# Optimization experiments

Hardware: AMD Instinct MI355X
Metric: run time of the kernel (lower is better)

Reference implementation:

```python
import jax, jax.numpy as jnp
import numpy as np

D_MODEL, N_HEADS = 1024, 16
HEAD_DIM = D_MODEL // N_HEADS  # 64
BS, Q_LEN, SEQ_LEN = 4, 1024, 1024


def setup_inputs() -> dict:
    key = jax.random.key(0)
    kq, kk, kv, kp, km = jax.random.split(key, 5)
    q = jax.random.normal(kq, (BS, N_HEADS, Q_LEN, HEAD_DIM), dtype=jnp.float32)
    k = jax.random.normal(kk, (BS, N_HEADS, HEAD_DIM, SEQ_LEN), dtype=jnp.float32)
    v = jax.random.normal(kv, (BS, N_HEADS, SEQ_LEN, HEAD_DIM), dtype=jnp.float32)
    prev = jax.random.normal(kp, (BS, N_HEADS, Q_LEN, SEQ_LEN), dtype=jnp.float32)
    attn_weighted_mask = jax.random.uniform(km, (1, N_HEADS, Q_LEN, SEQ_LEN), dtype=jnp.float32)
    scale = jnp.asarray(HEAD_DIM ** (-0.5), dtype=jnp.float32)  # nn.Parameter scalar
    return {"q": q, "k": k, "v": v, "prev": prev,
            "attn_weighted_mask": attn_weighted_mask, "scale": scale}


def reference(q, k, v, prev, attn_weighted_mask, scale):
    # scores = (q @ k) * scale + prev       [bs, h, q_len, seq_len]
    attn_scores = jnp.einsum('bhqd,bhds->bhqs', q, k) * scale + prev
    # softmax over keys; attn_dropout p=0.0 -> identity
    attn_weights = jax.nn.softmax(attn_scores, axis=-1)
    # post-softmax elementwise weighted mask
    attn_weights = attn_weights * attn_weighted_mask
    # output = attn_weights @ v             [bs, h, q_len, d_v]
    output = jnp.einsum('bhqs,bhsd->bhqd', attn_weights, v)
    # res_attention=True -> also return weights and pre-softmax scores
    return output, attn_weights, attn_scores
```

## Files before the change

kernel.cpp:

```cpp
#include <hip/hip_runtime.h>


#define QL 1024
#define SL 1024
#define HD 64

typedef __attribute__((ext_vector_type(8))) short bf16x8;
typedef __attribute__((ext_vector_type(4))) short bf16x4;
typedef __attribute__((ext_vector_type(4))) float f32x4;

__device__ __forceinline__ short f2bf(float f) {
    union { float f; unsigned u; } v; v.f = f;
    unsigned r = v.u + 0x7FFFu + ((v.u >> 16) & 1u);
    return (short)(r >> 16);
}

__global__ __launch_bounds__(256) void _prepack_kv(
    const float* __restrict__ k, const float* __restrict__ v,
    short* __restrict__ ws)
{
    __shared__ short tile[64][72];
    const int t = threadIdx.x;
    int b = blockIdx.x;
    const float* src; short* dst; int ld_src, ld_dst;
    if (b < 1024) {
        const int bh = b >> 4, st = b & 15;
        src = k + (size_t)bh * 65536 + st * 64;               ld_src = 1024;
        dst = ws + (size_t)bh * 65536 + (size_t)st * 4096;    ld_dst = 64;
    } else {
        b -= 1024;
        const int bh = b >> 4, st = b & 15;
        src = v + (size_t)bh * 65536 + (size_t)st * 4096;     ld_src = 64;
        dst = ws + 4194304 + (size_t)bh * 65536 + st * 64;    ld_dst = 1024;
    }
    {
        const int r = t >> 2, c0 = (t & 3) * 16;
#pragma unroll
        for (int i = 0; i < 4; ++i) {
            float4 f = *(const float4*)&src[(size_t)r * ld_src + c0 + 4 * i];
            bf16x4 s4 = { f2bf(f.x), f2bf(f.y), f2bf(f.z), f2bf(f.w) };
            *(bf16x4*)&tile[r][c0 + 4 * i] = s4;
        }
    }
    __syncthreads();
    {
        const int r = t >> 2, c0 = (t & 3) * 16;
        bf16x8 o0, o1;
#pragma unroll
        for (int j = 0; j < 8; ++j) o0[j] = tile[c0 + j][r];
#pragma unroll
        for (int j = 0; j < 8; ++j) o1[j] = tile[c0 + 8 + j][r];
        *(bf16x8*)&dst[(size_t)r * ld_dst + c0]     = o0;
        *(bf16x8*)&dst[(size_t)r * ld_dst + c0 + 8] = o1;
    }
}

__global__ __launch_bounds__(512, 4) void _attn_main(
    const float* __restrict__ q, const float* __restrict__ prev,
    const float* __restrict__ mask, const float* __restrict__ scale_p,
    const short* __restrict__ Kt, const short* __restrict__ Vt,
    float* __restrict__ out)
{
    __shared__ short wbuf[16384];
    __shared__ float red[128];
    __shared__ float obuf[1024];

    const int tid  = threadIdx.x;
    const int w    = tid >> 6;
    const int lane = tid & 63;
    const int quad = lane >> 4;
    const int lp   = lane & 15;

    const int j   = blockIdx.x;
    const int xcd = j & 7;
    const int i6  = j >> 3;
    const int bh  = xcd * 8 + (i6 >> 3);
    const int sub = i6 & 7;
    const int h   = bh & 15;

    const float scale = scale_p[0];

    const float* Qbh = q    + (size_t)bh * QL * HD;
    const float* Pbh = prev + (size_t)bh * QL * SL;
    const float* Mbh = mask + (size_t)h  * QL * SL;
    const short* Kb  = Kt + (size_t)bh * (SL * HD);
    const short* Vb  = Vt + (size_t)bh * (SL * HD);

    float* Obh = out            + (size_t)bh * QL * HD;
    float* Wbh = out + 4194304  + (size_t)bh * QL * SL;
    float* Sbh = out + 71303168 + (size_t)bh * QL * SL;

    const int s0   = 128 * w;
    const int sq   = s0 + quad * 4;
    const int dgrp = w & 3;
    const int kh   = w >> 2;

    f32x4 accA[8], accB[8];
    float4 qrA[4], qrB[4];

    {
        const int q0 = (sub * 8) * 16;
        const float* pp = Pbh + (size_t)(q0 + lp) * SL + sq;
#pragma unroll
        for (int t = 0; t < 8; ++t) accA[t] = *(const f32x4*)(pp + 16 * t);
        const float* qp = Qbh + (size_t)(q0 + lp) * HD + quad * 8;
        qrA[0] = *(const float4*)qp;        qrA[1] = *(const float4*)(qp + 4);
        qrA[2] = *(const float4*)(qp + 32); qrA[3] = *(const float4*)(qp + 36);
    }

    auto body = [&](f32x4 (&acc)[8], f32x4 (&accN)[8],
                    float4 (&qr)[4], float4 (&qrN)[4], int i) {
        const int q0  = (sub * 8 + i) * 16;
        const int iN  = (i < 7) ? i + 1 : i;
        const int q0N = (sub * 8 + iN) * 16;

        bf16x8 aq0, aq1;
        aq0[0] = f2bf(qr[0].x * scale); aq0[1] = f2bf(qr[0].y * scale);
        aq0[2] = f2bf(qr[0].z * scale); aq0[3] = f2bf(qr[0].w * scale);
        aq0[4] = f2bf(qr[1].x * scale); aq0[5] = f2bf(qr[1].y * scale);
        aq0[6] = f2bf(qr[1].z * scale); aq0[7] = f2bf(qr[1].w * scale);
        aq1[0] = f2bf(qr[2].x * scale); aq1[1] = f2bf(qr[2].y * scale);
        aq1[2] = f2bf(qr[2].z * scale); aq1[3] = f2bf(qr[2].w * scale);
        aq1[4] = f2bf(qr[3].x * scale); aq1[5] = f2bf(qr[3].y * scale);
        aq1[6] = f2bf(qr[3].z * scale); aq1[7] = f2bf(qr[3].w * scale);

#pragma unroll
        for (int t = 0; t < 8; ++t) {
            bf16x8 bk = *(const bf16x8*)&Kb[(size_t)(s0 + 16 * t + lp) * HD + quad * 8];
            acc[t] = __builtin_amdgcn_mfma_f32_16x16x32_bf16(bk, aq0, acc[t], 0, 0, 0);
        }
#pragma unroll
        for (int t = 0; t < 8; ++t) {
            bf16x8 bk = *(const bf16x8*)&Kb[(size_t)(s0 + 16 * t + lp) * HD + 32 + quad * 8];
            acc[t] = __builtin_amdgcn_mfma_f32_16x16x32_bf16(bk, aq1, acc[t], 0, 0, 0);
        }

        {
            float* sp = Sbh + (size_t)(q0 + lp) * SL + sq;
#pragma unroll
            for (int t = 0; t < 8; ++t) *(f32x4*)(sp + 16 * t) = acc[t];
        }

        {
            const float* pp = Pbh + (size_t)(q0N + lp) * SL + sq;
#pragma unroll
            for (int t = 0; t < 8; ++t) accN[t] = *(const f32x4*)(pp + 16 * t);
            const float* qp = Qbh + (size_t)(q0N + lp) * HD + quad * 8;
            qrN[0] = *(const float4*)qp;        qrN[1] = *(const float4*)(qp + 4);
            qrN[2] = *(const float4*)(qp + 32); qrN[3] = *(const float4*)(qp + 36);
        }

        float lsum = 0.f;
#pragma unroll
        for (int t = 0; t < 8; ++t) {
#pragma unroll
            for (int r = 0; r < 4; ++r) {
                float e = __expf(acc[t][r]);
                acc[t][r] = e;
                lsum += e;
            }
        }

        const float* mp = Mbh + (size_t)(q0 + lp) * SL + sq;
        float4 mkA[4];
#pragma unroll
        for (int t = 0; t < 4; ++t) mkA[t] = *(const float4*)(mp + 16 * t);

        lsum += __shfl_xor(lsum, 16);
        lsum += __shfl_xor(lsum, 32);
        if (lane < 16) red[w * 16 + lane] = lsum;
        __syncthreads();
        float rsum = 0.f;
#pragma unroll
        for (int u = 0; u < 8; ++u) rsum += red[u * 16 + lp];
        const float rinv = 1.0f / rsum;

        float4 mkB[4];
#pragma unroll
        for (int t = 0; t < 4; ++t) mkB[t] = *(const float4*)(mp + 64 + 16 * t);

        {
            float* wp = Wbh + (size_t)(q0 + lp) * SL + sq;
#pragma unroll
            for (int t = 0; t < 8; ++t) {
                float4 m4 = (t < 4) ? mkA[t] : mkB[t - 4];
                f32x4 wv;
#pragma unroll
                for (int r = 0; r < 4; ++r) wv[r] = acc[t][r] * rinv * m4[r];
                *(f32x4*)(wp + 16 * t) = wv;
                const int sb = sq + 16 * t;
                bf16x4 wb = { f2bf(wv[0]), f2bf(wv[1]), f2bf(wv[2]), f2bf(wv[3]) };
                *(bf16x4*)&wbuf[((sb >> 3) * 16 + lp) * 8 + (sb & 4)] = wb;
            }
        }
        __syncthreads();

        f32x4 oacc = {0.f, 0.f, 0.f, 0.f};
#pragma unroll 8
        for (int kk = 0; kk < 16; ++kk) {
            const int ks = kh * 16 + kk;
            bf16x8 aw = *(const bf16x8*)&wbuf[((ks * 4 + quad) * 16 + lp) * 8];
            bf16x8 bv = *(const bf16x8*)&Vb[(size_t)(16 * dgrp + lp) * SL
                                            + ks * 32 + quad * 8];
            oacc = __builtin_amdgcn_mfma_f32_16x16x32_bf16(bv, aw, oacc, 0, 0, 0);
        }
        if (kh == 1) {
            *(f32x4*)&obuf[lp * 64 + 16 * dgrp + quad * 4] = oacc;
        }
        __syncthreads();
        if (kh == 0) {
            f32x4 ov = *(const f32x4*)&obuf[lp * 64 + 16 * dgrp + quad * 4];
#pragma unroll
            for (int r = 0; r < 4; ++r) ov[r] += oacc[r];
            *(f32x4*)&Obh[(size_t)(q0 + lp) * HD + 16 * dgrp + quad * 4] = ov;
        }
    };

    for (int ii = 0; ii < 8; ii += 2) {
        body(accA, accB, qrA, qrB, ii);
        body(accB, accA, qrB, qrA, ii + 1);
    }
}

__global__ __launch_bounds__(256) void _attn_fallback(
    const float* __restrict__ q, const float* __restrict__ k,
    const float* __restrict__ v, const float* __restrict__ prev,
    const float* __restrict__ mask, const float* __restrict__ scale_p,
    float* __restrict__ out)
{
    const int WSTR = SL + 8;
    __shared__ short wbuf[16 * (SL + 8)];
    __shared__ float red[4 * 16];

    const int tid  = threadIdx.x;
    const int w    = tid >> 6;
    const int lane = tid & 63;
    const int quad = lane >> 4;
    const int lp   = lane & 15;

    const int blk = blockIdx.x;
    const int bh  = blk >> 6;
    const int qt  = blk & 63;
    const int h   = bh & 15;
    const int q0  = qt * 16;

    const float scale = scale_p[0];

    const float* Qb = q    + (size_t)bh * QL * HD + (size_t)q0 * HD;
    const float* Kb = k    + (size_t)bh * HD * SL;
    const float* Vb = v    + (size_t)bh * SL * HD;
    const float* Pb = prev + (size_t)bh * QL * SL + (size_t)q0 * SL;
    const float* Mb = mask + (size_t)h  * QL * SL + (size_t)q0 * SL;

    float* Ob   = out            + (size_t)bh * QL * HD + (size_t)q0 * HD;
    float* Wout = out + 4194304  + (size_t)bh * QL * SL + (size_t)q0 * SL;
    float* Sout = out + 71303168 + (size_t)bh * QL * SL + (size_t)q0 * SL;

    bf16x8 aq[2];
#pragma unroll
    for (int ks = 0; ks < 2; ++ks) {
        const float* qp = Qb + (size_t)lp * HD + ks * 32 + quad * 8;
#pragma unroll
        for (int j = 0; j < 8; ++j) aq[ks][j] = f2bf(qp[j] * scale);
    }

    const int s0 = 256 * w;
    f32x4 acc[16];
#pragma unroll
    for (int t = 0; t < 16; ++t) {
#pragma unroll
        for (int r = 0; r < 4; ++r)
            acc[t][r] = Pb[(size_t)(quad * 4 + r) * SL + s0 + 16 * t + lp];
    }
#pragma unroll
    for (int ks = 0; ks < 2; ++ks) {
#pragma unroll
        for (int t = 0; t < 16; ++t) {
            bf16x8 bk;
            const float* kp = Kb + (size_t)(ks * 32 + quad * 8) * SL + s0 + 16 * t + lp;
#pragma unroll
            for (int j = 0; j < 8; ++j) bk[j] = f2bf(kp[(size_t)j * SL]);
            acc[t] = __builtin_amdgcn_mfma_f32_16x16x32_bf16(aq[ks], bk, acc[t], 0, 0, 0);
        }
    }

    float lsum[4] = {0.f, 0.f, 0.f, 0.f};
#pragma unroll
    for (int t = 0; t < 16; ++t) {
#pragma unroll
        for (int r = 0; r < 4; ++r) {
            float sv = acc[t][r];
            Sout[(size_t)(quad * 4 + r) * SL + s0 + 16 * t + lp] = sv;
            float e = __expf(sv);
            acc[t][r] = e;
            lsum[r] += e;
        }
    }
#pragma unroll
    for (int r = 0; r < 4; ++r) {
        float s = lsum[r];
        s += __shfl_xor(s, 1);  s += __shfl_xor(s, 2);
        s += __shfl_xor(s, 4);  s += __shfl_xor(s, 8);
        lsum[r] = s;
    }
    if (lp == 0) {
#pragma unroll
        for (int r = 0; r < 4; ++r) red[w * 16 + quad * 4 + r] = lsum[r];
    }
    __syncthreads();
    float rinv[4];
#pragma unroll
    for (int r = 0; r < 4; ++r) {
        float s = red[0 * 16 + quad * 4 + r] + red[1 * 16 + quad * 4 + r]
                + red[2 * 16 + quad * 4 + r] + red[3 * 16 + quad * 4 + r];
        rinv[r] = 1.0f / s;
    }

#pragma unroll
    for (int t = 0; t < 16; ++t) {
#pragma unroll
        for (int r = 0; r < 4; ++r) {
            int row = quad * 4 + r;
            int col = s0 + 16 * t + lp;
            float wv = acc[t][r] * rinv[r] * Mb[(size_t)row * SL + col];
            Wout[(size_t)row * SL + col] = wv;
            wbuf[row * WSTR + col] = f2bf(wv);
        }
    }
    __syncthreads();

    f32x4 oacc = {0.f, 0.f, 0.f, 0.f};
#pragma unroll 4
    for (int ks = 0; ks < 32; ++ks) {
        bf16x8 aw = *(const bf16x8*)&wbuf[lp * WSTR + ks * 32 + quad * 8];
        bf16x8 bv;
        const float* vp = Vb + (size_t)(ks * 32 + quad * 8) * HD + 16 * w + lp;
#pragma unroll
        for (int j = 0; j < 8; ++j) bv[j] = f2bf(vp[(size_t)j * HD]);
        oacc = __builtin_amdgcn_mfma_f32_16x16x32_bf16(aw, bv, oacc, 0, 0, 0);
    }
#pragma unroll
    for (int r = 0; r < 4; ++r)
        Ob[(size_t)(quad * 4 + r) * HD + 16 * w + lp] = oacc[r];
}

extern "C" void kernel_launch(void* const* d_in, const int* in_sizes, int n_in,
                              void* d_out, int out_size, void* d_ws, size_t ws_size,
                              hipStream_t stream) {
    const float* q     = (const float*)d_in[0];
    const float* k     = (const float*)d_in[1];
    const float* v     = (const float*)d_in[2];
    const float* prev  = (const float*)d_in[3];
    const float* mask  = (const float*)d_in[4];
    const float* scale = (const float*)d_in[5];
    float* out = (float*)d_out;

    if (d_ws != nullptr && ws_size >= (size_t)16 * 1024 * 1024) {
        short* ws = (short*)d_ws;
        _prepack_kv<<<dim3(2048), dim3(256), 0, stream>>>(k, v, ws);
        _attn_main<<<dim3(512), dim3(512), 0, stream>>>(
            q, prev, mask, scale, ws, ws + 4194304, out);
    } else {
        _attn_fallback<<<dim3(4096), dim3(256), 0, stream>>>(
            q, k, v, prev, mask, scale, out);
    }
}
```

Baseline: 978.6 us.

## Remap blocks to heads per XCD, hoist mask loads, use LDS-only barriers

Changes the block-to-(batch, head) mapping so that blocks on the same XCD share a head and can reuse its mask rows in L2. Issues all mask loads before the next-tile prefetch, with a scheduling barrier to keep that order, and skips the redundant prefetch on the last iteration. Replaces __syncthreads with a barrier that waits only on LDS counters, so outstanding global loads and stores are no longer drained at each sync. The narrower barrier relies on correct waitcnt handling for global data used after the barrier.

```diff
diff --git a/kernel.cpp b/kernel.cpp
--- a/kernel.cpp
+++ b/kernel.cpp
@@ -14,6 +14,11 @@
     unsigned r = v.u + 0x7FFFu + ((v.u >> 16) & 1u);
     return (short)(r >> 16);
 }
+
+#define LDS_BAR() do {                                        \
+    asm volatile("s_waitcnt lgkmcnt(0)" ::: "memory");        \
+    __builtin_amdgcn_s_barrier();                             \
+} while (0)
 
 __global__ __launch_bounds__(256) void _prepack_kv(
     const float* __restrict__ k, const float* __restrict__ v,
@@ -72,11 +77,12 @@
     const int lp   = lane & 15;
 
     const int j   = blockIdx.x;
-    const int xcd = j & 7;
-    const int i6  = j >> 3;
-    const int bh  = xcd * 8 + (i6 >> 3);
-    const int sub = i6 & 7;
-    const int h   = bh & 15;
+    const int c   = j & 7;
+    const int m   = j >> 3;
+    const int sub = m & 7;
+    const int b   = m >> 4;
+    const int h   = ((m >> 3) & 1) * 8 + c;
+    const int bh  = b * 16 + h;
 
     const float scale = scale_p[0];
 
@@ -111,8 +117,7 @@
     auto body = [&](f32x4 (&acc)[8], f32x4 (&accN)[8],
                     float4 (&qr)[4], float4 (&qrN)[4], int i) {
         const int q0  = (sub * 8 + i) * 16;
-        const int iN  = (i < 7) ? i + 1 : i;
-        const int q0N = (sub * 8 + iN) * 16;
+        const int q0N = q0 + 16;
 
         bf16x8 aq0, aq1;
         aq0[0] = f2bf(qr[0].x * scale); aq0[1] = f2bf(qr[0].y * scale);
@@ -141,7 +146,16 @@
             for (int t = 0; t < 8; ++t) *(f32x4*)(sp + 16 * t) = acc[t];
         }
 
-        {
+        const float* mp = Mbh + (size_t)(q0 + lp) * SL + sq;
+        float4 mkA[4], mkB[4];
+#pragma unroll
+        for (int t = 0; t < 4; ++t) mkA[t] = *(const float4*)(mp + 16 * t);
+#pragma unroll
+        for (int t = 0; t < 4; ++t) mkB[t] = *(const float4*)(mp + 64 + 16 * t);
+
+        __builtin_amdgcn_sched_barrier(0);
+
+        if (i < 7) {
             const float* pp = Pbh + (size_t)(q0N + lp) * SL + sq;
 #pragma unroll
             for (int t = 0; t < 8; ++t) accN[t] = *(const f32x4*)(pp + 16 * t);
@@ -161,23 +175,14 @@
             }
         }
 
-        const float* mp = Mbh + (size_t)(q0 + lp) * SL + sq;
-        float4 mkA[4];
-#pragma unroll
-        for (int t = 0; t < 4; ++t) mkA[t] = *(const float4*)(mp + 16 * t);
-
         lsum += __shfl_xor(lsum, 16);
         lsum += __shfl_xor(lsum, 32);
         if (lane < 16) red[w * 16 + lane] = lsum;
-        __syncthreads();
+        LDS_BAR();
         float rsum = 0.f;
 #pragma unroll
         for (int u = 0; u < 8; ++u) rsum += red[u * 16 + lp];
         const float rinv = 1.0f / rsum;
-
-        float4 mkB[4];
-#pragma unroll
-        for (int t = 0; t < 4; ++t) mkB[t] = *(const float4*)(mp + 64 + 16 * t);
 
         {
             float* wp = Wbh + (size_t)(q0 + lp) * SL + sq;
@@ -193,7 +198,7 @@
                 *(bf16x4*)&wbuf[((sb >> 3) * 16 + lp) * 8 + (sb & 4)] = wb;
             }
         }
-        __syncthreads();
+        LDS_BAR();
 
         f32x4 oacc = {0.f, 0.f, 0.f, 0.f};
 #pragma unroll 8
@@ -207,7 +212,7 @@
         if (kh == 1) {
             *(f32x4*)&obuf[lp * 64 + 16 * dgrp + quad * 4] = oacc;
         }
-        __syncthreads();
+        LDS_BAR();
         if (kh == 0) {
             f32x4 ov = *(const f32x4*)&obuf[lp * 64 + 16 * dgrp + quad * 4];
 #pragma unroll
```

Measured after the change: 1.047 ms. 1.07x slower.

## Remap blocks to share mask tiles across batches and reuse loaded mask rows

Applied to the files above, without the earlier changes.

Changes the block-to-work mapping so each block handles one head and two 16-row query tiles across all four batch elements, instead of eight query tiles of a single (batch, head). The mask tile depends only on head and query rows, so it is now loaded once per query tile and reused for the four batches, cutting mask reads about fourfold. The cost is keeping the mask values in registers across iterations, which raises register pressure under the 512x4 launch bounds. Per-iteration K/V pointers also switch between batches, which may reduce L2 locality for K and V.

```diff
diff --git a/kernel.cpp b/kernel.cpp
--- a/kernel.cpp
+++ b/kernel.cpp
@@ -72,23 +72,14 @@
     const int lp   = lane & 15;
 
     const int j   = blockIdx.x;
-    const int xcd = j & 7;
-    const int i6  = j >> 3;
-    const int bh  = xcd * 8 + (i6 >> 3);
-    const int sub = i6 & 7;
-    const int h   = bh & 15;
+    const int c   = j & 7;
+    const int r   = j >> 3;
+    const int h   = c + 8 * (r & 1);
+    const int q0b = (r >> 1) * 32;
 
     const float scale = scale_p[0];
 
-    const float* Qbh = q    + (size_t)bh * QL * HD;
-    const float* Pbh = prev + (size_t)bh * QL * SL;
-    const float* Mbh = mask + (size_t)h  * QL * SL;
-    const short* Kb  = Kt + (size_t)bh * (SL * HD);
-    const short* Vb  = Vt + (size_t)bh * (SL * HD);
-
-    float* Obh = out            + (size_t)bh * QL * HD;
-    float* Wbh = out + 4194304  + (size_t)bh * QL * SL;
-    float* Sbh = out + 71303168 + (size_t)bh * QL * SL;
+    const float* Mbh = mask + (size_t)h * QL * SL;
 
     const int s0   = 128 * w;
     const int sq   = s0 + quad * 4;
@@ -97,22 +88,29 @@
 
     f32x4 accA[8], accB[8];
     float4 qrA[4], qrB[4];
+    float4 mkA[4], mkB[4];
 
     {
-        const int q0 = (sub * 8) * 16;
-        const float* pp = Pbh + (size_t)(q0 + lp) * SL + sq;
+        const int bh0 = h;
+        const float* pp = prev + (size_t)bh0 * QL * SL + (size_t)(q0b + lp) * SL + sq;
 #pragma unroll
         for (int t = 0; t < 8; ++t) accA[t] = *(const f32x4*)(pp + 16 * t);
-        const float* qp = Qbh + (size_t)(q0 + lp) * HD + quad * 8;
+        const float* qp = q + (size_t)bh0 * QL * HD + (size_t)(q0b + lp) * HD + quad * 8;
         qrA[0] = *(const float4*)qp;        qrA[1] = *(const float4*)(qp + 4);
         qrA[2] = *(const float4*)(qp + 32); qrA[3] = *(const float4*)(qp + 36);
     }
 
     auto body = [&](f32x4 (&acc)[8], f32x4 (&accN)[8],
                     float4 (&qr)[4], float4 (&qrN)[4], int i) {
-        const int q0  = (sub * 8 + i) * 16;
-        const int iN  = (i < 7) ? i + 1 : i;
-        const int q0N = (sub * 8 + iN) * 16;
+        const int b   = i & 3;
+        const int bh  = b * 16 + h;
+        const int q0  = q0b + ((i >> 2) << 4);
+
+        const short* Kb = Kt + (size_t)bh * (SL * HD);
+        const short* Vb = Vt + (size_t)bh * (SL * HD);
+        float* Obh = out            + (size_t)bh * QL * HD;
+        float* Wbh = out + 4194304  + (size_t)bh * QL * SL;
+        float* Sbh = out + 71303168 + (size_t)bh * QL * SL;
 
         bf16x8 aq0, aq1;
         aq0[0] = f2bf(qr[0].x * scale); aq0[1] = f2bf(qr[0].y * scale);
@@ -141,11 +139,22 @@
             for (int t = 0; t < 8; ++t) *(f32x4*)(sp + 16 * t) = acc[t];
         }
 
-        {
-            const float* pp = Pbh + (size_t)(q0N + lp) * SL + sq;
+        if ((i & 3) == 0) {
+            const float* mp = Mbh + (size_t)(q0 + lp) * SL + sq;
+#pragma unroll
+            for (int t = 0; t < 4; ++t) mkA[t] = *(const float4*)(mp + 16 * t);
+#pragma unroll
+            for (int t = 0; t < 4; ++t) mkB[t] = *(const float4*)(mp + 64 + 16 * t);
+        }
+
+        if (i < 7) {
+            const int bN  = (i + 1) & 3;
+            const int bhN = bN * 16 + h;
+            const int q0N = q0b + (((i + 1) >> 2) << 4);
+            const float* pp = prev + (size_t)bhN * QL * SL + (size_t)(q0N + lp) * SL + sq;
 #pragma unroll
             for (int t = 0; t < 8; ++t) accN[t] = *(const f32x4*)(pp + 16 * t);
-            const float* qp = Qbh + (size_t)(q0N + lp) * HD + quad * 8;
+            const float* qp = q + (size_t)bhN * QL * HD + (size_t)(q0N + lp) * HD + quad * 8;
             qrN[0] = *(const float4*)qp;        qrN[1] = *(const float4*)(qp + 4);
             qrN[2] = *(const float4*)(qp + 32); qrN[3] = *(const float4*)(qp + 36);
         }
@@ -154,17 +163,12 @@
 #pragma unroll
         for (int t = 0; t < 8; ++t) {
 #pragma unroll
-            for (int r = 0; r < 4; ++r) {
-                float e = __expf(acc[t][r]);
-                acc[t][r] = e;
+            for (int rr = 0; rr < 4; ++rr) {
+                float e = __expf(acc[t][rr]);
+                acc[t][rr] = e;
                 lsum += e;
             }
         }
-
-        const float* mp = Mbh + (size_t)(q0 + lp) * SL + sq;
-        float4 mkA[4];
-#pragma unroll
-        for (int t = 0; t < 4; ++t) mkA[t] = *(const float4*)(mp + 16 * t);
 
         lsum += __shfl_xor(lsum, 16);
         lsum += __shfl_xor(lsum, 32);
@@ -175,10 +179,6 @@
         for (int u = 0; u < 8; ++u) rsum += red[u * 16 + lp];
         const float rinv = 1.0f / rsum;
 
-        float4 mkB[4];
-#pragma unroll
-        for (int t = 0; t < 4; ++t) mkB[t] = *(const float4*)(mp + 64 + 16 * t);
-
         {
             float* wp = Wbh + (size_t)(q0 + lp) * SL + sq;
 #pragma unroll
@@ -186,7 +186,7 @@
                 float4 m4 = (t < 4) ? mkA[t] : mkB[t - 4];
                 f32x4 wv;
 #pragma unroll
-                for (int r = 0; r < 4; ++r) wv[r] = acc[t][r] * rinv * m4[r];
+                for (int rr = 0; rr < 4; ++rr) wv[rr] = acc[t][rr] * rinv * m4[rr];
                 *(f32x4*)(wp + 16 * t) = wv;
                 const int sb = sq + 16 * t;
                 bf16x4 wb = { f2bf(wv[0]), f2bf(wv[1]), f2bf(wv[2]), f2bf(wv[3]) };
@@ -211,7 +211,7 @@
         if (kh == 0) {
             f32x4 ov = *(const f32x4*)&obuf[lp * 64 + 16 * dgrp + quad * 4];
 #pragma unroll
-            for (int r = 0; r < 4; ++r) ov[r] += oacc[r];
+            for (int rr = 0; rr < 4; ++rr) ov[rr] += oacc[rr];
             *(f32x4*)&Obh[(size_t)(q0 + lp) * HD + 16 * dgrp + quad * 4] = ov;
         }
     };
@@ -261,7 +261,7 @@
     for (int ks = 0; ks < 2; ++ks) {
         const float* qp = Qb + (size_t)lp * HD + ks * 32 + quad * 8;
 #pragma unroll
-        for (int j = 0; j < 8; ++j) aq[ks][j] = f2bf(qp[j] * scale);
+        for (int jj = 0; jj < 8; ++jj) aq[ks][jj] = f2bf(qp[jj] * scale);
     }
 
     const int s0 = 256 * w;
@@ -279,7 +279,7 @@
             bf16x8 bk;
             const float* kp = Kb + (size_t)(ks * 32 + quad * 8) * SL + s0 + 16 * t + lp;
 #pragma unroll
-            for (int j = 0; j < 8; ++j) bk[j] = f2bf(kp[(size_t)j * SL]);
+            for (int jj = 0; jj < 8; ++jj) bk[jj] = f2bf(kp[(size_t)jj * SL]);
             acc[t] = __builtin_amdgcn_mfma_f32_16x16x32_bf16(aq[ks], bk, acc[t], 0, 0, 0);
         }
     }
@@ -336,7 +336,7 @@
         bf16x8 bv;
         const float* vp = Vb + (size_t)(ks * 32 + quad * 8) * HD + 16 * w + lp;
 #pragma unroll
-        for (int j = 0; j < 8; ++j) bv[j] = f2bf(vp[(size_t)j * HD]);
+        for (int jj = 0; jj < 8; ++jj) bv[jj] = f2bf(vp[(size_t)jj * HD]);
         oacc = __builtin_amdgcn_mfma_f32_16x16x32_bf16(aw, bv, oacc, 0, 0, 0);
     }
 #pragma unroll
```

Measured after the change: 991.8 us. Within noise of the previous version (+1.4%).
